# Kernel tuning notes

Measured on AMD Instinct MI355X. Metric: run time of the kernel, lower is better.

The kernel has to match this reference:

```python
import jax, jax.numpy as jnp
import numpy as np

B, T, D = 2, 2048, 2048
H, KV, HD = 16, 4, 128
EPS = 1e-6


def _rmsnorm(x, scale):
    # flax.linen.RMSNorm over last axis: x / sqrt(mean(x^2) + eps) * scale
    var = jnp.mean(jnp.square(x), axis=-1, keepdims=True)
    return x * jax.lax.rsqrt(var + EPS) * scale


def _rope(x, cos, sin):
    # x: [b, t, h, d]; cos/sin: [t, d]
    x_rot = jnp.stack([-x[..., 1::2], x[..., 0::2]], axis=-1)
    x_rot = x_rot.reshape(*x_rot.shape[:-2], -1)
    return x * cos[None, :, None, :] + x_rot * sin[None, :, None, :]


def setup_inputs() -> dict:
    key = jax.random.key(0)
    ks = jax.random.split(key, 5)
    x = jax.random.normal(ks[0], (B, T, D), jnp.float32)
    Wq = jax.random.normal(ks[1], (D, H * HD), jnp.float32) / np.sqrt(D)
    Wk = jax.random.normal(ks[2], (D, KV * HD), jnp.float32) / np.sqrt(D)
    Wv = jax.random.normal(ks[3], (D, KV * HD), jnp.float32) / np.sqrt(D)
    Wo = jax.random.normal(ks[4], (H * HD, D), jnp.float32) / np.sqrt(H * HD)
    q_scale = jnp.ones((HD,), jnp.float32)
    k_scale = jnp.ones((HD,), jnp.float32)
    # standard RoPE tables, interleaved-pair convention
    pos = jnp.arange(T, dtype=jnp.float32)
    inv_freq = 1.0 / (10000.0 ** (jnp.arange(0, HD, 2, dtype=jnp.float32) / HD))
    freqs = pos[:, None] * inv_freq[None, :]  # [T, HD/2]
    cos = jnp.repeat(jnp.cos(freqs), 2, axis=-1)  # [T, HD]
    sin = jnp.repeat(jnp.sin(freqs), 2, axis=-1)
    mask = jnp.tril(jnp.ones((T, T), bool))[None, None]  # causal [1,1,T,T]
    return {"x": x, "Wq": Wq, "Wk": Wk, "Wv": Wv, "Wo": Wo,
            "q_scale": q_scale, "k_scale": k_scale,
            "cos": cos, "sin": sin, "mask": mask}


def reference(x, Wq, Wk, Wv, Wo, q_scale, k_scale, cos, sin, mask):
    num_groups = H // KV
    q = (x @ Wq).reshape(B, T, H, HD)
    k = (x @ Wk).reshape(B, T, KV, HD)
    v = (x @ Wv).reshape(B, T, KV, HD)
    q = _rmsnorm(q, q_scale)
    k = _rmsnorm(k, k_scale)
    q = _rope(q, cos, sin)
    k = _rope(k, cos, sin)
    k = jnp.repeat(k, num_groups, axis=2)  # [b, t, H, d]
    v = jnp.repeat(v, num_groups, axis=2)
    scores = jnp.einsum('bqhd,bkhd->bhqk', q, k) / jnp.sqrt(jnp.float32(HD))
    scores = jnp.where(mask, scores, jnp.finfo(scores.dtype).min)
    attn = jax.nn.softmax(scores, axis=-1)
    out = jnp.einsum('bhqk,bkhd->bqhd', attn, v)
    out = out.reshape(B, T, H * HD)
    return out @ Wo
```

## Files before the change

### kernel.cpp

```cpp
#include <hip/hip_runtime.h>
#include <hip/hip_bf16.h>

#define B_   2
#define T_   2048
#define D_   2048
#define H_   16
#define KV_  4
#define HD_  128
#define BT_  (B_*T_)
#define QKVP 3072
#define KOFF 2048
#define VOFF 2560
static constexpr float EPS_ = 1e-6f;

typedef unsigned short u16;
typedef __attribute__((ext_vector_type(8))) short short8;
typedef __attribute__((ext_vector_type(4))) float f32x4;
typedef __attribute__((ext_vector_type(4))) unsigned short u16x4;

__device__ __forceinline__ u16 f2bf(float f){
    unsigned u = __float_as_uint(f);
    u += 0x7FFF + ((u >> 16) & 1);
    return (u16)(u >> 16);
}
__device__ __forceinline__ float bf2f(u16 u){
    return __uint_as_float((unsigned)u << 16);
}

__device__ __forceinline__ void async_copy16(const void* g, void* l) {
    __builtin_amdgcn_global_load_lds(
        (const __attribute__((address_space(1))) unsigned int*)g,
        (__attribute__((address_space(3))) unsigned int*)l, 16, 0, 0);
}

__global__ __launch_bounds__(256) void cvt_f32_bf16_kernel(
    const float* __restrict__ in, u16* __restrict__ out, int n)
{
    const int i = (blockIdx.x*256 + threadIdx.x)*4;
    if (i < n) {
        float4 v = *(const float4*)&in[i];
        u16x4 w = { f2bf(v.x), f2bf(v.y), f2bf(v.z), f2bf(v.w) };
        *(u16x4*)&out[i] = w;
    }
}

__global__ __launch_bounds__(256) void transpose_cvt_kernel(
    const float* __restrict__ in, u16* __restrict__ out, int R, int C)
{
    __shared__ u16 tile[64][65];
    const int r0 = blockIdx.y*64, c0 = blockIdx.x*64;
    const int tr = threadIdx.x >> 4;
    const int tc = (threadIdx.x & 15) * 4;
    #pragma unroll
    for (int i = 0; i < 4; i++) {
        const int r = tr + i*16;
        float4 v = *(const float4*)&in[(size_t)(r0 + r)*C + c0 + tc];
        tile[tc+0][r] = f2bf(v.x);
        tile[tc+1][r] = f2bf(v.y);
        tile[tc+2][r] = f2bf(v.z);
        tile[tc+3][r] = f2bf(v.w);
    }
    __syncthreads();
    #pragma unroll
    for (int i = 0; i < 4; i++) {
        const int c = tr + i*16;
        u16x4 w = { tile[c][tc+0], tile[c][tc+1], tile[c][tc+2], tile[c][tc+3] };
        *(u16x4*)&out[(size_t)(c0 + c)*R + r0 + tc] = w;
    }
}

__global__ __launch_bounds__(256) void transpose_v_kernel(
    const u16* __restrict__ qkv, u16* __restrict__ vt)
{
    __shared__ u16 tile[64][65];
    const int t0 = blockIdx.x*64;
    const int d0 = blockIdx.y*64;
    const int bk = blockIdx.z;
    const int tr = threadIdx.x >> 4;
    const int tc = (threadIdx.x & 15) * 4;
    #pragma unroll
    for (int i = 0; i < 4; i++) {
        const int t = t0 + tr + i*16;
        u16x4 v = *(const u16x4*)&qkv[(size_t)((bk>>2)*T_ + t)*QKVP + VOFF
                                      + (bk&3)*HD_ + d0 + tc];
        tile[tc+0][tr+i*16] = v[0];
        tile[tc+1][tr+i*16] = v[1];
        tile[tc+2][tr+i*16] = v[2];
        tile[tc+3][tr+i*16] = v[3];
    }
    __syncthreads();
    #pragma unroll
    for (int i = 0; i < 4; i++) {
        const int d = tr + i*16;
        u16x4 w = { tile[d][tc+0], tile[d][tc+1], tile[d][tc+2], tile[d][tc+3] };
        *(u16x4*)&vt[((size_t)bk*HD_ + d0 + d)*T_ + t0 + tc] = w;
    }
}

#define GBM 128
#define GBN 128
#define GBK 32

template<bool OUT_BF16>
__global__ __launch_bounds__(256) void gemm_mfma_kernel(
    const u16* __restrict__ A, const u16* __restrict__ Bt,
    void* __restrict__ C, int N, int K, int lda, int ldb, int ldc)
{
    __shared__ __align__(16) u16 As[GBM][GBK];
    __shared__ __align__(16) u16 Bs[GBN][GBK];
    const int tid  = threadIdx.x;
    const int lane = tid & 63;
    const int wave = tid >> 6;
    const int l15  = lane & 15;
    const int quad = lane >> 4;
    const int wr   = (wave >> 1) * 64;
    const int wc   = (wave & 1) * 64;
    const size_t row0 = (size_t)blockIdx.y * GBM;
    const size_t col0 = (size_t)blockIdx.x * GBN;

    f32x4 acc[4][4];
    #pragma unroll
    for (int i = 0; i < 4; i++)
        #pragma unroll
        for (int j = 0; j < 4; j++)
            acc[i][j] = (f32x4){0.f,0.f,0.f,0.f};

    for (int k0 = 0; k0 < K; k0 += GBK) {
        #pragma unroll
        for (int c = 0; c < 2; c++) {
            const int e = (c*256 + tid) * 8;
            const int r = e >> 5, cc = e & 31;
            async_copy16(A  + (row0 + r)*lda + k0 + cc, &As[r][cc]);
            async_copy16(Bt + (col0 + r)*ldb + k0 + cc, &Bs[r][cc]);
        }
        __syncthreads();

        short8 af[4], bf[4];
        #pragma unroll
        for (int i = 0; i < 4; i++)
            af[i] = *(const short8*)&As[wr + i*16 + l15][quad*8];
        #pragma unroll
        for (int j = 0; j < 4; j++)
            bf[j] = *(const short8*)&Bs[wc + j*16 + l15][quad*8];
        #pragma unroll
        for (int i = 0; i < 4; i++)
            #pragma unroll
            for (int j = 0; j < 4; j++)
                acc[i][j] = __builtin_amdgcn_mfma_f32_16x16x32_bf16(
                    af[i], bf[j], acc[i][j], 0, 0, 0);
        __syncthreads();
    }

    #pragma unroll
    for (int i = 0; i < 4; i++)
        #pragma unroll
        for (int r = 0; r < 4; r++) {
            const size_t row = row0 + wr + i*16 + quad*4 + r;
            #pragma unroll
            for (int j = 0; j < 4; j++) {
                const size_t col = col0 + wc + j*16 + l15;
                if (OUT_BF16) ((u16*)C)[row*ldc + col] = f2bf(acc[i][j][r]);
                else          ((float*)C)[row*ldc + col] = acc[i][j][r];
            }
        }
}

__global__ __launch_bounds__(256) void rmsnorm_rope_kernel(
    u16* __restrict__ qk, const float* __restrict__ scale,
    const float* __restrict__ cosT, const float* __restrict__ sinT,
    int heads_per_token, int head_off, float post_scale)
{
    const int wid   = blockIdx.x*4 + (threadIdx.x >> 6);
    const int lane  = threadIdx.x & 63;
    const int token = wid / heads_per_token;
    const int hidx  = wid % heads_per_token;
    const int t     = token & (T_ - 1);
    u16* p = qk + (size_t)token*QKVP + head_off + hidx*HD_ + lane*2;

    const unsigned u = *(const unsigned*)p;
    const float x0 = bf2f((u16)(u & 0xffff));
    const float x1 = bf2f((u16)(u >> 16));
    float ss = x0*x0 + x1*x1;
    #pragma unroll
    for (int off = 32; off > 0; off >>= 1) ss += __shfl_xor(ss, off);
    const float rms = rsqrtf(ss * (1.0f/HD_) + EPS_);

    const float2 sc = *(const float2*)&scale[lane*2];
    const float2 cs = *(const float2*)&cosT[(size_t)t*HD_ + lane*2];
    const float2 sn = *(const float2*)&sinT[(size_t)t*HD_ + lane*2];
    const float n0 = x0 * rms * sc.x;
    const float n1 = x1 * rms * sc.y;
    const float r0 = (n0*cs.x - n1*sn.x) * post_scale;
    const float r1 = (n1*cs.y + n0*sn.y) * post_scale;
    *(unsigned*)p = (unsigned)f2bf(r0) | ((unsigned)f2bf(r1) << 16);
}

#define BQ  64
#define BKV 64

__global__ __launch_bounds__(256, 2) void attn_mfma6_kernel(
    const u16* __restrict__ qkv, const u16* __restrict__ Vtg)
{
    __shared__ __align__(16) u16 Ks[2][16][BKV][8];
    __shared__ __align__(16) u16 Vt[2][8][HD_][8];
    __shared__ __align__(16) u16 Pb[4][8][16][8];

    const int pr   = blockIdx.x;
    const int h    = blockIdx.y;
    const int b    = blockIdx.z;
    const int kvh  = h >> 2;
    const int tid  = threadIdx.x;
    const int lane = tid & 63;
    const int wave = tid >> 6;
    const int l15  = lane & 15;
    const int quad = lane >> 4;
    const int NT   = T_ / BQ;

    for (int phase = 0; phase < 2; phase++) {
        const int qt = phase ? pr : (NT - 1 - pr);
        const int q0 = qt * BQ;

        short8 qf[4];
        {
            const u16* qbase = qkv + (size_t)(b*T_ + q0 + wave*16 + l15)*QKVP + h*HD_;
            #pragma unroll
            for (int kt = 0; kt < 4; kt++)
                qf[kt] = *(const short8*)(qbase + (kt*4 + quad)*8);
        }

        float lsum[4] = {0.f, 0.f, 0.f, 0.f};
        f32x4 oacc[8];
        #pragma unroll
        for (int cv = 0; cv < 8; cv++) oacc[cv] = (f32x4){0.f,0.f,0.f,0.f};

        const int ntiles = qt + 1;

        #pragma unroll
        for (int it = 0; it < 4; it++) {
            const int n   = it*256 + tid;
            const int cc  = n >> 6;
            const int key = n & 63;
            async_copy16(qkv + (size_t)(b*T_ + key)*QKVP + KOFF + kvh*HD_ + cc*8,
                         &Ks[0][cc][key][0]);
        }
        #pragma unroll
        for (int it = 0; it < 4; it++) {
            const int n  = it*256 + tid;
            const int cc = n >> 7;
            const int d  = n & 127;
            async_copy16(Vtg + ((size_t)(b*KV_ + kvh)*HD_ + d)*T_ + cc*8,
                         &Vt[0][cc][d][0]);
        }
        __syncthreads();

        int cur = 0;
        for (int t = 0; t < ntiles; t++) {
            if (t + 1 < ntiles) {
                const int k0n = (t + 1) * BKV;
                #pragma unroll
                for (int it = 0; it < 4; it++) {
                    const int n   = it*256 + tid;
                    const int cc  = n >> 6;
                    const int key = n & 63;
                    async_copy16(qkv + (size_t)(b*T_ + k0n + key)*QKVP + KOFF + kvh*HD_ + cc*8,
                                 &Ks[cur^1][cc][key][0]);
                }
                #pragma unroll
                for (int it = 0; it < 4; it++) {
                    const int n  = it*256 + tid;
                    const int cc = n >> 7;
                    const int d  = n & 127;
                    async_copy16(Vtg + ((size_t)(b*KV_ + kvh)*HD_ + d)*T_ + k0n + cc*8,
                                 &Vt[cur^1][cc][d][0]);
                }
            }

            const int k0 = t * BKV;

            f32x4 s[4];
            #pragma unroll
            for (int c = 0; c < 4; c++) s[c] = (f32x4){0.f,0.f,0.f,0.f};
            __builtin_amdgcn_s_setprio(1);
            #pragma unroll
            for (int kt = 0; kt < 4; kt++) {
                #pragma unroll
                for (int c = 0; c < 4; c++) {
                    short8 bf = *(const short8*)&Ks[cur][kt*4 + quad][c*16 + l15][0];
                    s[c] = __builtin_amdgcn_mfma_f32_16x16x32_bf16(qf[kt], bf, s[c], 0, 0, 0);
                }
            }
            __builtin_amdgcn_s_setprio(0);

            if (t == ntiles - 1) {
                const int qrow0 = q0 + wave*16 + quad*4;
                #pragma unroll
                for (int r = 0; r < 4; r++)
                    #pragma unroll
                    for (int c = 0; c < 4; c++) {
                        const int key = k0 + c*16 + l15;
                        if (key > qrow0 + r) s[c][r] = -1e30f;
                    }
            }
            #pragma unroll
            for (int r = 0; r < 4; r++)
                #pragma unroll
                for (int c = 0; c < 4; c++) {
                    const float p = __expf(s[c][r]);
                    s[c][r] = p;
                    lsum[r] += p;
                }

            #pragma unroll
            for (int r = 0; r < 4; r++)
                #pragma unroll
                for (int c = 0; c < 4; c++)
                    Pb[wave][c*2 + (l15 >> 3)][quad*4 + r][l15 & 7] = f2bf(s[c][r]);

            __builtin_amdgcn_s_setprio(1);
            #pragma unroll
            for (int kt2 = 0; kt2 < 2; kt2++) {
                short8 a = *(const short8*)&Pb[wave][kt2*4 + quad][l15][0];
                #pragma unroll
                for (int cv = 0; cv < 8; cv++) {
                    short8 vf = *(const short8*)&Vt[cur][kt2*4 + quad][cv*16 + l15][0];
                    oacc[cv] = __builtin_amdgcn_mfma_f32_16x16x32_bf16(a, vf, oacc[cv], 0, 0, 0);
                }
            }
            __builtin_amdgcn_s_setprio(0);

            __syncthreads();
            cur ^= 1;
        }

        #pragma unroll
        for (int r = 0; r < 4; r++) {
            float tot = lsum[r];
            #pragma unroll
            for (int off = 1; off < 16; off <<= 1)
                tot += __shfl_xor(tot, off, 16);
            const float linv = 1.0f / tot;
            u16* orow = (u16*)qkv + (size_t)(b*T_ + q0 + wave*16 + quad*4 + r)*QKVP
                        + h*HD_ + l15;
            #pragma unroll
            for (int cv = 0; cv < 8; cv++)
                orow[cv*16] = f2bf(oacc[cv][r] * linv);
        }
    }
}

extern "C" void kernel_launch(void* const* d_in, const int* in_sizes, int n_in,
                              void* d_out, int out_size, void* d_ws, size_t ws_size,
                              hipStream_t stream)
{
    const float* x    = (const float*)d_in[0];
    const float* Wq   = (const float*)d_in[1];
    const float* Wk   = (const float*)d_in[2];
    const float* Wv   = (const float*)d_in[3];
    const float* Wo   = (const float*)d_in[4];
    const float* qsc  = (const float*)d_in[5];
    const float* ksc  = (const float*)d_in[6];
    const float* cosT = (const float*)d_in[7];
    const float* sinT = (const float*)d_in[8];
    float* out = (float*)d_out;

    u16* xb     = (u16*)d_ws;
    u16* Wqkvt  = xb    + (size_t)BT_*D_;
    u16* Wot    = Wqkvt + (size_t)QKVP*D_;
    u16* qkv    = Wot   + (size_t)D_*(H_*HD_);
    u16* vtg    = qkv   + (size_t)BT_*QKVP;

    cvt_f32_bf16_kernel<<<(BT_*D_)/1024, 256, 0, stream>>>(x, xb, BT_*D_);
    transpose_cvt_kernel<<<dim3((H_*HD_)/64,  D_/64), 256, 0, stream>>>(
        Wq, Wqkvt, D_, H_*HD_);
    transpose_cvt_kernel<<<dim3((KV_*HD_)/64, D_/64), 256, 0, stream>>>(
        Wk, Wqkvt + (size_t)KOFF*D_, D_, KV_*HD_);
    transpose_cvt_kernel<<<dim3((KV_*HD_)/64, D_/64), 256, 0, stream>>>(
        Wv, Wqkvt + (size_t)VOFF*D_, D_, KV_*HD_);
    transpose_cvt_kernel<<<dim3(D_/64, (H_*HD_)/64),  256, 0, stream>>>(
        Wo, Wot, H_*HD_, D_);

    gemm_mfma_kernel<true><<<dim3(QKVP/GBN, BT_/GBM), 256, 0, stream>>>(
        xb, Wqkvt, qkv, QKVP, D_, D_, D_, QKVP);

    rmsnorm_rope_kernel<<<(BT_*H_)/4,  256, 0, stream>>>(
        qkv, qsc, cosT, sinT, H_, 0, 0.08838834764831845f);
    rmsnorm_rope_kernel<<<(BT_*KV_)/4, 256, 0, stream>>>(
        qkv, ksc, cosT, sinT, KV_, KOFF, 1.0f);

    transpose_v_kernel<<<dim3(T_/64, HD_/64, B_*KV_), 256, 0, stream>>>(qkv, vtg);

    attn_mfma6_kernel<<<dim3(T_/BQ/2, H_, B_), 256, 0, stream>>>(qkv, vtg);

    gemm_mfma_kernel<false><<<dim3(D_/GBN, BT_/GBM), 256, 0, stream>>>(
        qkv, Wot, out, D_, D_, QKVP, D_, D_);
}
```

Baseline: 375.3 us.

## Split attention waves into 2x2 query-row/key-column tiles with shared P buffer

Reorganizes the attention kernel's four waves from each owning 16 query rows into a 2x2 grid: each wave handles 32 query rows and half of the keys (for QK^T) or half of the head dim (for PV). Each K and V fragment loaded from LDS now feeds two MFMAs, which roughly halves LDS reads per MFMA. The cost is that P has to be shared across waves through a padded LDS buffer, which needs an extra block barrier per tile. Row sums are also combined across key halves via LDS at the end, adding two more syncs per phase.

```diff
diff --git a/kernel.cpp b/kernel.cpp
--- a/kernel.cpp
+++ b/kernel.cpp
@@ -198,12 +198,13 @@
 #define BQ  64
 #define BKV 64
 
-__global__ __launch_bounds__(256, 2) void attn_mfma6_kernel(
+__global__ __launch_bounds__(256, 2) void attn_mfma7_kernel(
     const u16* __restrict__ qkv, const u16* __restrict__ Vtg)
 {
     __shared__ __align__(16) u16 Ks[2][16][BKV][8];
     __shared__ __align__(16) u16 Vt[2][8][HD_][8];
-    __shared__ __align__(16) u16 Pb[4][8][16][8];
+    __shared__ __align__(16) u16 Pb[64][88];
+    __shared__ float SumX[2][64];
 
     const int pr   = blockIdx.x;
     const int h    = blockIdx.y;
@@ -212,6 +213,8 @@
     const int tid  = threadIdx.x;
     const int lane = tid & 63;
     const int wave = tid >> 6;
+    const int rh   = wave >> 1;
+    const int kh   = wave & 1;
     const int l15  = lane & 15;
     const int quad = lane >> 4;
     const int NT   = T_ / BQ;
@@ -220,18 +223,25 @@
         const int qt = phase ? pr : (NT - 1 - pr);
         const int q0 = qt * BQ;
 
-        short8 qf[4];
-        {
-            const u16* qbase = qkv + (size_t)(b*T_ + q0 + wave*16 + l15)*QKVP + h*HD_;
+        short8 qf[2][4];
+        #pragma unroll
+        for (int rf = 0; rf < 2; rf++) {
+            const u16* qbase = qkv + (size_t)(b*T_ + q0 + rh*32 + rf*16 + l15)*QKVP + h*HD_;
             #pragma unroll
             for (int kt = 0; kt < 4; kt++)
-                qf[kt] = *(const short8*)(qbase + (kt*4 + quad)*8);
-        }
-
-        float lsum[4] = {0.f, 0.f, 0.f, 0.f};
-        f32x4 oacc[8];
-        #pragma unroll
-        for (int cv = 0; cv < 8; cv++) oacc[cv] = (f32x4){0.f,0.f,0.f,0.f};
+                qf[rf][kt] = *(const short8*)(qbase + kt*32 + quad*8);
+        }
+
+        float lsum[2][4];
+        #pragma unroll
+        for (int rf = 0; rf < 2; rf++)
+            #pragma unroll
+            for (int r = 0; r < 4; r++) lsum[rf][r] = 0.f;
+        f32x4 oacc[2][4];
+        #pragma unroll
+        for (int rf = 0; rf < 2; rf++)
+            #pragma unroll
+            for (int cv = 0; cv < 4; cv++) oacc[rf][cv] = (f32x4){0.f,0.f,0.f,0.f};
 
         const int ntiles = qt + 1;
 
@@ -277,53 +287,67 @@
 
             const int k0 = t * BKV;
 
-            f32x4 s[4];
-            #pragma unroll
-            for (int c = 0; c < 4; c++) s[c] = (f32x4){0.f,0.f,0.f,0.f};
+            f32x4 s[2][2];
+            #pragma unroll
+            for (int rf = 0; rf < 2; rf++)
+                #pragma unroll
+                for (int cj = 0; cj < 2; cj++) s[rf][cj] = (f32x4){0.f,0.f,0.f,0.f};
             __builtin_amdgcn_s_setprio(1);
             #pragma unroll
             for (int kt = 0; kt < 4; kt++) {
                 #pragma unroll
-                for (int c = 0; c < 4; c++) {
-                    short8 bf = *(const short8*)&Ks[cur][kt*4 + quad][c*16 + l15][0];
-                    s[c] = __builtin_amdgcn_mfma_f32_16x16x32_bf16(qf[kt], bf, s[c], 0, 0, 0);
+                for (int cj = 0; cj < 2; cj++) {
+                    short8 kf = *(const short8*)&Ks[cur][kt*4 + quad][kh*32 + cj*16 + l15][0];
+                    #pragma unroll
+                    for (int rf = 0; rf < 2; rf++)
+                        s[rf][cj] = __builtin_amdgcn_mfma_f32_16x16x32_bf16(
+                            qf[rf][kt], kf, s[rf][cj], 0, 0, 0);
                 }
             }
             __builtin_amdgcn_s_setprio(0);
 
             if (t == ntiles - 1) {
-                const int qrow0 = q0 + wave*16 + quad*4;
+                #pragma unroll
+                for (int rf = 0; rf < 2; rf++) {
+                    const int qrow0 = q0 + rh*32 + rf*16 + quad*4;
+                    #pragma unroll
+                    for (int r = 0; r < 4; r++)
+                        #pragma unroll
+                        for (int cj = 0; cj < 2; cj++) {
+                            const int key = k0 + kh*32 + cj*16 + l15;
+                            if (key > qrow0 + r) s[rf][cj][r] = -1e30f;
+                        }
+                }
+            }
+            #pragma unroll
+            for (int rf = 0; rf < 2; rf++)
                 #pragma unroll
                 for (int r = 0; r < 4; r++)
                     #pragma unroll
-                    for (int c = 0; c < 4; c++) {
-                        const int key = k0 + c*16 + l15;
-                        if (key > qrow0 + r) s[c][r] = -1e30f;
+                    for (int cj = 0; cj < 2; cj++) {
+                        const float p = __expf(s[rf][cj][r]);
+                        s[rf][cj][r] = p;
+                        lsum[rf][r] += p;
+                        Pb[rh*32 + rf*16 + quad*4 + r][kh*32 + cj*16 + l15] = f2bf(p);
                     }
-            }
-            #pragma unroll
-            for (int r = 0; r < 4; r++)
-                #pragma unroll
-                for (int c = 0; c < 4; c++) {
-                    const float p = __expf(s[c][r]);
-                    s[c][r] = p;
-                    lsum[r] += p;
-                }
-
-            #pragma unroll
-            for (int r = 0; r < 4; r++)
-                #pragma unroll
-                for (int c = 0; c < 4; c++)
-                    Pb[wave][c*2 + (l15 >> 3)][quad*4 + r][l15 & 7] = f2bf(s[c][r]);
+
+            asm volatile("s_waitcnt lgkmcnt(0)" ::: "memory");
+            __builtin_amdgcn_s_barrier();
 
             __builtin_amdgcn_s_setprio(1);
             #pragma unroll
             for (int kt2 = 0; kt2 < 2; kt2++) {
-                short8 a = *(const short8*)&Pb[wave][kt2*4 + quad][l15][0];
-                #pragma unroll
-                for (int cv = 0; cv < 8; cv++) {
-                    short8 vf = *(const short8*)&Vt[cur][kt2*4 + quad][cv*16 + l15][0];
-                    oacc[cv] = __builtin_amdgcn_mfma_f32_16x16x32_bf16(a, vf, oacc[cv], 0, 0, 0);
+                short8 pa[2];
+                #pragma unroll
+                for (int rf = 0; rf < 2; rf++)
+                    pa[rf] = *(const short8*)&Pb[rh*32 + rf*16 + l15][kt2*32 + quad*8];
+                #pragma unroll
+                for (int cv = 0; cv < 4; cv++) {
+                    short8 vf = *(const short8*)&Vt[cur][kt2*4 + quad][kh*64 + cv*16 + l15][0];
+                    #pragma unroll
+                    for (int rf = 0; rf < 2; rf++)
+                        oacc[rf][cv] = __builtin_amdgcn_mfma_f32_16x16x32_bf16(
+                            pa[rf], vf, oacc[rf][cv], 0, 0, 0);
                 }
             }
             __builtin_amdgcn_s_setprio(0);
@@ -333,18 +357,29 @@
         }
 
         #pragma unroll
-        for (int r = 0; r < 4; r++) {
-            float tot = lsum[r];
-            #pragma unroll
-            for (int off = 1; off < 16; off <<= 1)
-                tot += __shfl_xor(tot, off, 16);
-            const float linv = 1.0f / tot;
-            u16* orow = (u16*)qkv + (size_t)(b*T_ + q0 + wave*16 + quad*4 + r)*QKVP
-                        + h*HD_ + l15;
-            #pragma unroll
-            for (int cv = 0; cv < 8; cv++)
-                orow[cv*16] = f2bf(oacc[cv][r] * linv);
-        }
+        for (int rf = 0; rf < 2; rf++)
+            #pragma unroll
+            for (int r = 0; r < 4; r++) {
+                float tot = lsum[rf][r];
+                #pragma unroll
+                for (int off = 1; off < 16; off <<= 1)
+                    tot += __shfl_xor(tot, off, 16);
+                if (l15 == 0) SumX[kh][rh*32 + rf*16 + quad*4 + r] = tot;
+            }
+        __syncthreads();
+        #pragma unroll
+        for (int rf = 0; rf < 2; rf++)
+            #pragma unroll
+            for (int r = 0; r < 4; r++) {
+                const int rIdx = rh*32 + rf*16 + quad*4 + r;
+                const float linv = 1.0f / (SumX[0][rIdx] + SumX[1][rIdx]);
+                u16* orow = (u16*)qkv + (size_t)(b*T_ + q0 + rIdx)*QKVP
+                            + h*HD_ + kh*64 + l15;
+                #pragma unroll
+                for (int cv = 0; cv < 4; cv++)
+                    orow[cv*16] = f2bf(oacc[rf][cv][r] * linv);
+            }
+        __syncthreads();
     }
 }
 
@@ -389,7 +424,7 @@
 
     transpose_v_kernel<<<dim3(T_/64, HD_/64, B_*KV_), 256, 0, stream>>>(qkv, vtg);
 
-    attn_mfma6_kernel<<<dim3(T_/BQ/2, H_, B_), 256, 0, stream>>>(qkv, vtg);
+    attn_mfma7_kernel<<<dim3(T_/BQ/2, H_, B_), 256, 0, stream>>>(qkv, vtg);
 
     gemm_mfma_kernel<false><<<dim3(D_/GBN, BT_/GBM), 256, 0, stream>>>(
         qkv, Wot, out, D_, D_, QKVP, D_, D_);
```

Result: no change. 379.1 us (+1.0%).

## Drop KV double-buffering and q-tile pairing in favor of higher attention occupancy

Applied to the files above, without the earlier changes.

The attention kernel no longer processes a pair of causal q-tiles per block and no longer double-buffers the K/V tiles in shared memory. Instead it launches one block per q-tile, in reverse order so the longest tiles start first, loads each K/V tile synchronously, and raises the launch-bounds minimum to 4 blocks per CU. The aim is to hide memory latency through more resident waves and a smaller LDS footprint rather than software prefetch. In exchange, each block stalls on every tile load, and the grid relies on the hardware scheduler to balance the causal workload.

```diff
diff --git a/kernel.cpp b/kernel.cpp
--- a/kernel.cpp
+++ b/kernel.cpp
@@ -198,14 +198,14 @@
 #define BQ  64
 #define BKV 64
 
-__global__ __launch_bounds__(256, 2) void attn_mfma6_kernel(
+__global__ __launch_bounds__(256, 4) void attn_mfma8_kernel(
     const u16* __restrict__ qkv, const u16* __restrict__ Vtg)
 {
-    __shared__ __align__(16) u16 Ks[2][16][BKV][8];
-    __shared__ __align__(16) u16 Vt[2][8][HD_][8];
+    __shared__ __align__(16) u16 Ks[16][BKV][8];
+    __shared__ __align__(16) u16 Vt[8][HD_][8];
     __shared__ __align__(16) u16 Pb[4][8][16][8];
 
-    const int pr   = blockIdx.x;
+    const int qt   = (T_/BQ - 1) - blockIdx.x;
     const int h    = blockIdx.y;
     const int b    = blockIdx.z;
     const int kvh  = h >> 2;
@@ -214,137 +214,108 @@
     const int wave = tid >> 6;
     const int l15  = lane & 15;
     const int quad = lane >> 4;
-    const int NT   = T_ / BQ;
-
-    for (int phase = 0; phase < 2; phase++) {
-        const int qt = phase ? pr : (NT - 1 - pr);
-        const int q0 = qt * BQ;
-
-        short8 qf[4];
-        {
-            const u16* qbase = qkv + (size_t)(b*T_ + q0 + wave*16 + l15)*QKVP + h*HD_;
-            #pragma unroll
-            for (int kt = 0; kt < 4; kt++)
-                qf[kt] = *(const short8*)(qbase + (kt*4 + quad)*8);
-        }
-
-        float lsum[4] = {0.f, 0.f, 0.f, 0.f};
-        f32x4 oacc[8];
-        #pragma unroll
-        for (int cv = 0; cv < 8; cv++) oacc[cv] = (f32x4){0.f,0.f,0.f,0.f};
-
-        const int ntiles = qt + 1;
+    const int q0   = qt * BQ;
+
+    short8 qf[4];
+    {
+        const u16* qbase = qkv + (size_t)(b*T_ + q0 + wave*16 + l15)*QKVP + h*HD_;
+        #pragma unroll
+        for (int kt = 0; kt < 4; kt++)
+            qf[kt] = *(const short8*)(qbase + (kt*4 + quad)*8);
+    }
+
+    float lsum[4] = {0.f, 0.f, 0.f, 0.f};
+    f32x4 oacc[8];
+    #pragma unroll
+    for (int cv = 0; cv < 8; cv++) oacc[cv] = (f32x4){0.f,0.f,0.f,0.f};
+
+    const int ntiles = qt + 1;
+    for (int t = 0; t < ntiles; t++) {
+        const int k0 = t * BKV;
+        __syncthreads();
 
         #pragma unroll
         for (int it = 0; it < 4; it++) {
             const int n   = it*256 + tid;
             const int cc  = n >> 6;
             const int key = n & 63;
-            async_copy16(qkv + (size_t)(b*T_ + key)*QKVP + KOFF + kvh*HD_ + cc*8,
-                         &Ks[0][cc][key][0]);
+            async_copy16(qkv + (size_t)(b*T_ + k0 + key)*QKVP + KOFF + kvh*HD_ + cc*8,
+                         &Ks[cc][key][0]);
         }
         #pragma unroll
         for (int it = 0; it < 4; it++) {
             const int n  = it*256 + tid;
             const int cc = n >> 7;
             const int d  = n & 127;
-            async_copy16(Vtg + ((size_t)(b*KV_ + kvh)*HD_ + d)*T_ + cc*8,
-                         &Vt[0][cc][d][0]);
+            async_copy16(Vtg + ((size_t)(b*KV_ + kvh)*HD_ + d)*T_ + k0 + cc*8,
+                         &Vt[cc][d][0]);
         }
         __syncthreads();
 
-        int cur = 0;
-        for (int t = 0; t < ntiles; t++) {
-            if (t + 1 < ntiles) {
-                const int k0n = (t + 1) * BKV;
-                #pragma unroll
-                for (int it = 0; it < 4; it++) {
-                    const int n   = it*256 + tid;
-                    const int cc  = n >> 6;
-                    const int key = n & 63;
-                    async_copy16(qkv + (size_t)(b*T_ + k0n + key)*QKVP + KOFF + kvh*HD_ + cc*8,
-                                 &Ks[cur^1][cc][key][0]);
-                }
-                #pragma unroll
-                for (int it = 0; it < 4; it++) {
-                    const int n  = it*256 + tid;
-                    const int cc = n >> 7;
-                    const int d  = n & 127;
-                    async_copy16(Vtg + ((size_t)(b*KV_ + kvh)*HD_ + d)*T_ + k0n + cc*8,
-                                 &Vt[cur^1][cc][d][0]);
-                }
+        f32x4 s[4];
+        #pragma unroll
+        for (int c = 0; c < 4; c++) s[c] = (f32x4){0.f,0.f,0.f,0.f};
+        __builtin_amdgcn_s_setprio(1);
+        #pragma unroll
+        for (int kt = 0; kt < 4; kt++) {
+            #pragma unroll
+            for (int c = 0; c < 4; c++) {
+                short8 bf = *(const short8*)&Ks[kt*4 + quad][c*16 + l15][0];
+                s[c] = __builtin_amdgcn_mfma_f32_16x16x32_bf16(qf[kt], bf, s[c], 0, 0, 0);
             }
-
-            const int k0 = t * BKV;
-
-            f32x4 s[4];
-            #pragma unroll
-            for (int c = 0; c < 4; c++) s[c] = (f32x4){0.f,0.f,0.f,0.f};
-            __builtin_amdgcn_s_setprio(1);
-            #pragma unroll
-            for (int kt = 0; kt < 4; kt++) {
-                #pragma unroll
-                for (int c = 0; c < 4; c++) {
-                    short8 bf = *(const short8*)&Ks[cur][kt*4 + quad][c*16 + l15][0];
-                    s[c] = __builtin_amdgcn_mfma_f32_16x16x32_bf16(qf[kt], bf, s[c], 0, 0, 0);
-                }
-            }
-            __builtin_amdgcn_s_setprio(0);
-
-            if (t == ntiles - 1) {
-                const int qrow0 = q0 + wave*16 + quad*4;
-                #pragma unroll
-                for (int r = 0; r < 4; r++)
-                    #pragma unroll
-                    for (int c = 0; c < 4; c++) {
-                        const int key = k0 + c*16 + l15;
-                        if (key > qrow0 + r) s[c][r] = -1e30f;
-                    }
-            }
+        }
+        __builtin_amdgcn_s_setprio(0);
+
+        if (t == ntiles - 1) {
+            const int qrow0 = q0 + wave*16 + quad*4;
             #pragma unroll
             for (int r = 0; r < 4; r++)
                 #pragma unroll
                 for (int c = 0; c < 4; c++) {
-                    const float p = __expf(s[c][r]);
-                    s[c][r] = p;
-                    lsum[r] += p;
+                    const int key = k0 + c*16 + l15;
+                    if (key > qrow0 + r) s[c][r] = -1e30f;
                 }
-
-            #pragma unroll
-            for (int r = 0; r < 4; r++)
-                #pragma unroll
-                for (int c = 0; c < 4; c++)
-                    Pb[wave][c*2 + (l15 >> 3)][quad*4 + r][l15 & 7] = f2bf(s[c][r]);
-
-            __builtin_amdgcn_s_setprio(1);
-            #pragma unroll
-            for (int kt2 = 0; kt2 < 2; kt2++) {
-                short8 a = *(const short8*)&Pb[wave][kt2*4 + quad][l15][0];
-                #pragma unroll
-                for (int cv = 0; cv < 8; cv++) {
-                    short8 vf = *(const short8*)&Vt[cur][kt2*4 + quad][cv*16 + l15][0];
-                    oacc[cv] = __builtin_amdgcn_mfma_f32_16x16x32_bf16(a, vf, oacc[cv], 0, 0, 0);
-                }
+        }
+        #pragma unroll
+        for (int r = 0; r < 4; r++)
+            #pragma unroll
+            for (int c = 0; c < 4; c++) {
+                const float p = __expf(s[c][r]);
+                s[c][r] = p;
+                lsum[r] += p;
             }
-            __builtin_amdgcn_s_setprio(0);
-
-            __syncthreads();
-            cur ^= 1;
-        }
-
-        #pragma unroll
-        for (int r = 0; r < 4; r++) {
-            float tot = lsum[r];
-            #pragma unroll
-            for (int off = 1; off < 16; off <<= 1)
-                tot += __shfl_xor(tot, off, 16);
-            const float linv = 1.0f / tot;
-            u16* orow = (u16*)qkv + (size_t)(b*T_ + q0 + wave*16 + quad*4 + r)*QKVP
-                        + h*HD_ + l15;
-            #pragma unroll
-            for (int cv = 0; cv < 8; cv++)
-                orow[cv*16] = f2bf(oacc[cv][r] * linv);
-        }
+
+        #pragma unroll
+        for (int r = 0; r < 4; r++)
+            #pragma unroll
+            for (int c = 0; c < 4; c++)
+                Pb[wave][c*2 + (l15 >> 3)][quad*4 + r][l15 & 7] = f2bf(s[c][r]);
+
+        __builtin_amdgcn_s_setprio(1);
+        #pragma unroll
+        for (int kt2 = 0; kt2 < 2; kt2++) {
+            short8 a = *(const short8*)&Pb[wave][kt2*4 + quad][l15][0];
+            #pragma unroll
+            for (int cv = 0; cv < 8; cv++) {
+                short8 vf = *(const short8*)&Vt[kt2*4 + quad][cv*16 + l15][0];
+                oacc[cv] = __builtin_amdgcn_mfma_f32_16x16x32_bf16(a, vf, oacc[cv], 0, 0, 0);
+            }
+        }
+        __builtin_amdgcn_s_setprio(0);
+    }
+
+    #pragma unroll
+    for (int r = 0; r < 4; r++) {
+        float tot = lsum[r];
+        #pragma unroll
+        for (int off = 1; off < 16; off <<= 1)
+            tot += __shfl_xor(tot, off, 16);
+        const float linv = 1.0f / tot;
+        u16* orow = (u16*)qkv + (size_t)(b*T_ + q0 + wave*16 + quad*4 + r)*QKVP
+                    + h*HD_ + l15;
+        #pragma unroll
+        for (int cv = 0; cv < 8; cv++)
+            orow[cv*16] = f2bf(oacc[cv][r] * linv);
     }
 }
 
@@ -389,7 +360,7 @@
 
     transpose_v_kernel<<<dim3(T_/64, HD_/64, B_*KV_), 256, 0, stream>>>(qkv, vtg);
 
-    attn_mfma6_kernel<<<dim3(T_/BQ/2, H_, B_), 256, 0, stream>>>(qkv, vtg);
+    attn_mfma8_kernel<<<dim3(T_/BQ, H_, B_), 256, 0, stream>>>(qkv, vtg);
 
     gemm_mfma_kernel<false><<<dim3(D_/GBN, BT_/GBM), 256, 0, stream>>>(
         qkv, Wot, out, D_, D_, QKVP, D_, D_);
```

After: 438.9 us. 17.0% more time.
